# Kernel tuning notes

Measured on AMD Instinct MI355X. Metric: run time of the kernel, lower is better.

The kernel has to match this reference:

```python
import jax, jax.numpy as jnp
import numpy as np

B, S, D, H, FF = 4, 1024, 1024, 8, 4096
DK = D // H
EPS = 1e-5


def layernorm(x, g, b):
    m = jnp.mean(x, axis=-1, keepdims=True)
    v = jnp.mean(jnp.square(x - m), axis=-1, keepdims=True)
    return (x - m) * jax.lax.rsqrt(v + EPS) * g + b


def setup_inputs() -> dict:
    key = jax.random.key(0)
    ks = jax.random.split(key, 8)
    w = lambda k, shape: jax.random.normal(k, shape, jnp.float32) * 0.02
    return {
        "x": jax.random.normal(ks[0], (B, S, D), jnp.float32),
        "mask": jnp.ones((B, 1, 1, S), jnp.int32),  # unused in 'infer' mode, kept for fidelity
        "g1": jnp.ones((D,), jnp.float32), "b1": jnp.zeros((D,), jnp.float32),
        "Wq": w(ks[1], (D, D)), "bq": jnp.zeros((D,), jnp.float32),
        "Wk": w(ks[2], (D, D)), "bk": jnp.zeros((D,), jnp.float32),
        "Wv": w(ks[3], (D, H * D)), "bv": jnp.zeros((H * D,), jnp.float32),
        "g2": jnp.ones((D,), jnp.float32), "b2": jnp.zeros((D,), jnp.float32),
        "W1": w(ks[4], (D, FF)), "bw1": jnp.zeros((FF,), jnp.float32),
        "W2": w(ks[5], (FF, D)), "bw2": jnp.zeros((D,), jnp.float32),
    }


def reference(x, mask, g1, b1, Wq, bq, Wk, bk, Wv, bv, g2, b2, W1, bw1, W2, bw2):
    # --- MultiHeadedAttention (mode='infer'; mask is ignored by this path) ---
    xn = layernorm(x, g1, b1)                                   # [B,S,D]
    q = (xn @ Wq + bq).reshape(B, S, H, DK).transpose(0, 2, 1, 3)  # [B,H,S,DK]
    k = (xn @ Wk + bk).reshape(B, S, H, DK).transpose(0, 2, 1, 3)  # [B,H,S,DK]
    v = (xn @ Wv + bv).reshape(B, S, H, D).transpose(0, 2, 1, 3)   # [B,H,S,D]
    scores = jnp.einsum('bhqd,bhkd->bhqk', q, k) / jnp.sqrt(jnp.float32(DK))
    p = jax.nn.softmax(scores, axis=-1)                          # [B,H,S,S]
    ctx = jnp.einsum('bhqk,bhkd->bhqd', p, v)                    # [B,H,S,D]
    # Source does x.view(-1, B, dim, h).sum(heads).view(B, S, dim) on the
    # contiguous [B,H,S,D] tensor: a raw row-major reshape, reproduced exactly.
    attn_out = ctx.reshape(S, B, D, H).sum(axis=-1).reshape(B, S, D)
    # --- residual + SublayerConnection (pre-norm GELU FFN) ---
    x1 = x + attn_out
    xn2 = layernorm(x1, g2, b2)
    ffn = jax.nn.gelu(xn2 @ W1 + bw1, approximate=False) @ W2 + bw2
    return x1 + ffn
```

## Files before the change

kernel.cpp:

```cpp
#include <hip/hip_runtime.h>
#include <hip/hip_bf16.h>
#include <math.h>

typedef __attribute__((ext_vector_type(8))) short   short8;
typedef __attribute__((ext_vector_type(4))) short   short4v;
typedef __attribute__((ext_vector_type(8))) __bf16  bf16x8;
typedef __attribute__((ext_vector_type(4))) float   f32x4;

typedef const __attribute__((address_space(1))) void cgv_t;
typedef __attribute__((address_space(3))) void lv_t;

__device__ __forceinline__ float bs2f(short s) {
  unsigned int u = ((unsigned int)(unsigned short)s) << 16;
  return __builtin_bit_cast(float, u);
}
__device__ __forceinline__ short f2bs(float f) {
  __hip_bfloat16 h = __float2bfloat16(f);
  return __builtin_bit_cast(short, h);
}
__device__ __forceinline__ void glds16(const short* g, short* l) {
  __builtin_amdgcn_global_load_lds((cgv_t*)g, (lv_t*)l, 16, 0, 0);
}


__global__ __launch_bounds__(256) void transpose_k(const float* __restrict__ in,
                                                   short* __restrict__ out,
                                                   int R, int C) {
  __shared__ __align__(16) short T[64 * 72];
  const int r0 = blockIdx.y * 64, c0 = blockIdx.x * 64;
  const int t = threadIdx.x;
  {
    const int rr = t >> 4;
    const int cc = (t & 15) << 2;
#pragma unroll
    for (int h = 0; h < 4; h++) {
      const int row = rr + h * 16;
      f32x4 v = *(const f32x4*)(in + (long)(r0 + row) * C + c0 + cc);
#pragma unroll
      for (int e = 0; e < 4; e++) T[row * 72 + cc + e] = f2bs(v[e]);
    }
  }
  __syncthreads();
  {
    const int cr = t >> 3;
    const int rs = (t & 7) << 3;
#pragma unroll
    for (int h = 0; h < 2; h++) {
      const int c = cr + h * 32;
      short8 v;
#pragma unroll
      for (int e = 0; e < 8; e++) v[e] = T[(rs + e) * 72 + c];
      *(short8*)(out + (long)(c0 + c) * R + r0 + rs) = v;
    }
  }
}

__global__ __launch_bounds__(256) void wv8_k(const float* __restrict__ Wv,
                                             short* __restrict__ out) {
  __shared__ __align__(16) short T[64 * 72];
  const int r0 = blockIdx.x * 64, k0 = blockIdx.y * 64;
  const int t = threadIdx.x;
  const int wave = t >> 6, lane = t & 63;
  const int r = r0 + lane;
#pragma unroll 4
  for (int i = 0; i < 16; i++) {
    const int k = k0 + wave * 16 + i;
    const float* src = Wv + (long)k * 8192 + 8 * r;
    f32x4 a = *(const f32x4*)src;
    f32x4 b = *(const f32x4*)(src + 4);
    float s = (a[0] + a[1] + a[2] + a[3]) + (b[0] + b[1] + b[2] + b[3]);
    T[lane * 72 + wave * 16 + i] = f2bs(s);
  }
  __syncthreads();
  const int rr = t >> 3, kc = (t & 7) << 3;
#pragma unroll
  for (int half = 0; half < 2; half++) {
    const int rl = rr + half * 32;
    *(short8*)(out + (long)(r0 + rl) * 1024 + k0 + kc) = *(const short8*)&T[rl * 72 + kc];
  }
}

__global__ __launch_bounds__(256) void bv8_k(const float* __restrict__ bv,
                                             float* __restrict__ out) {
  const int r = blockIdx.x * 256 + threadIdx.x;
  f32x4 a = *(const f32x4*)(bv + 8 * r);
  f32x4 b = *(const f32x4*)(bv + 8 * r + 4);
  out[r] = (a[0] + a[1] + a[2] + a[3]) + (b[0] + b[1] + b[2] + b[3]);
}

__global__ __launch_bounds__(256) void ln_k(const float* __restrict__ in,
                                            const float* __restrict__ g,
                                            const float* __restrict__ b,
                                            short* __restrict__ out) {
  const int t = threadIdx.x;
  const long base = (long)blockIdx.x * 1024 + t * 4;
  f32x4 f = *(const f32x4*)(in + base);
  float v[4] = {f[0], f[1], f[2], f[3]};
  float s1 = v[0] + v[1] + v[2] + v[3];
  float s2 = v[0]*v[0] + v[1]*v[1] + v[2]*v[2] + v[3]*v[3];
#pragma unroll
  for (int off = 32; off; off >>= 1) {
    s1 += __shfl_xor(s1, off);
    s2 += __shfl_xor(s2, off);
  }
  __shared__ float rs[4], rq[4];
  if ((t & 63) == 0) { rs[t >> 6] = s1; rq[t >> 6] = s2; }
  __syncthreads();
  s1 = rs[0] + rs[1] + rs[2] + rs[3];
  s2 = rq[0] + rq[1] + rq[2] + rq[3];
  const float mean = s1 * (1.0f / 1024.0f);
  const float var  = s2 * (1.0f / 1024.0f) - mean * mean;
  const float rstd = rsqrtf(var + 1e-5f);
  f32x4 gv = *(const f32x4*)(g + t * 4);
  f32x4 bv = *(const f32x4*)(b + t * 4);
  short4v o;
#pragma unroll
  for (int i = 0; i < 4; i++)
    o[i] = f2bs((v[i] - mean) * rstd * gv[i] + bv[i]);
  *(short4v*)(out + base) = o;
}

__global__ __launch_bounds__(256) void reduce4_k(const float* __restrict__ p,
                                                 const float* __restrict__ x1,
                                                 const float* __restrict__ bias,
                                                 float* __restrict__ out) {
  const int t = threadIdx.x;
  const long base = (long)blockIdx.x * 1024 + t * 4;
  f32x4 a = *(const f32x4*)(p + base);
  f32x4 b = *(const f32x4*)(p + 4194304 + base);
  f32x4 c = *(const f32x4*)(p + 8388608 + base);
  f32x4 d = *(const f32x4*)(p + 12582912 + base);
  f32x4 e = *(const f32x4*)(x1 + base);
  f32x4 g = *(const f32x4*)(bias + t * 4);
  *(f32x4*)(out + base) = a + b + c + d + e + g;
}

__global__ __launch_bounds__(256, 2) void flash_k(
    const short* __restrict__ Qg_, const short* __restrict__ Kg_,
    const short* __restrict__ V8T, const float* __restrict__ xg,
    float* __restrict__ x1) {
  __shared__ __align__(16) short smem[40960];
  short* Qs = smem;
  short* Ks = smem + 8192;
  short* Vs = smem + 24576;

  const int t = threadIdx.x;
  const int wave = t >> 6, lane = t & 63;
  const int llo = lane & 15, lhi = lane >> 4;

  int lin = blockIdx.x + (blockIdx.y << 4);
  lin = (lin & 7) * 64 + (lin >> 3);
  const int q0 = (lin & 15) * 64;
  const int bh = lin >> 4, b = bh >> 3, h = bh & 7;

  const short* Qg = Qg_ + ((long)(b * 1024 + q0)) * 1024 + h * 128;
  const short* Kg = Kg_ + ((long)b * 1024) * 1024 + h * 128;
  const short* Vg = V8T + (long)bh * 131072;

  const int srow = t >> 2;
  const int sgc = (((t & 3) ^ ((t >> 3) & 3)) << 3);
  const int wbase = wave * 512;
  const int swzo = ((lhi ^ ((llo >> 1) & 3)) << 3);
  const int arow = (wave * 16 + llo) * 32 + swzo;

#pragma unroll
  for (int kk = 0; kk < 4; kk++)
    glds16(Qg + (long)srow * 1024 + kk * 32 + sgc, Qs + kk * 2048 + wbase);

  f32x4 o[8];
  float mR[4], lR[4];
#pragma unroll
  for (int i = 0; i < 8; i++) o[i] = f32x4{0.f, 0.f, 0.f, 0.f};
#pragma unroll
  for (int r = 0; r < 4; r++) { mR[r] = -1e30f; lR[r] = 0.f; }

  for (int it = 0; it < 8; it++) {
    const int kt0 = it * 128;
#pragma unroll
    for (int kk = 0; kk < 4; kk++) {
      glds16(Kg + (long)(kt0 + srow) * 1024 + kk * 32 + sgc,
             Ks + kk * 4096 + wbase);
      glds16(Kg + (long)(kt0 + 64 + srow) * 1024 + kk * 32 + sgc,
             Ks + kk * 4096 + 2048 + wbase);
      glds16(Vg + (long)srow * 1024 + kt0 + kk * 32 + sgc,
             Vs + kk * 4096 + wbase);
      glds16(Vg + (long)(64 + srow) * 1024 + kt0 + kk * 32 + sgc,
             Vs + kk * 4096 + 2048 + wbase);
    }
    __syncthreads();

    f32x4 s[8];
#pragma unroll
    for (int i = 0; i < 8; i++) s[i] = f32x4{0.f, 0.f, 0.f, 0.f};
#pragma unroll
    for (int kk = 0; kk < 4; kk++) {
      bf16x8 aq = *(const bf16x8*)(Qs + kk * 2048 + arow);
#pragma unroll
      for (int ct = 0; ct < 8; ct++) {
        bf16x8 bk = *(const bf16x8*)(Ks + kk * 4096 + (ct * 16 + llo) * 32 + swzo);
        s[ct] = __builtin_amdgcn_mfma_f32_16x16x32_bf16(aq, bk, s[ct], 0, 0, 0);
      }
    }
    float mt[4];
#pragma unroll
    for (int r = 0; r < 4; r++) {
      float m = s[0][r];
#pragma unroll
      for (int ct = 1; ct < 8; ct++) m = fmaxf(m, s[ct][r]);
      m = fmaxf(m, __shfl_xor(m, 1));
      m = fmaxf(m, __shfl_xor(m, 2));
      m = fmaxf(m, __shfl_xor(m, 4));
      m = fmaxf(m, __shfl_xor(m, 8));
      mt[r] = m;
    }
    bool need = (mt[0] > mR[0] + 8.f) | (mt[1] > mR[1] + 8.f) |
                (mt[2] > mR[2] + 8.f) | (mt[3] > mR[3] + 8.f);
    if (__any(need)) {
      float alpha[4];
#pragma unroll
      for (int r = 0; r < 4; r++) {
        const float mn = fmaxf(mR[r], mt[r]);
        alpha[r] = __builtin_amdgcn_exp2f(mR[r] - mn);
        mR[r] = mn;
        lR[r] *= alpha[r];
      }
#pragma unroll
      for (int ct = 0; ct < 8; ct++)
#pragma unroll
        for (int r = 0; r < 4; r++) o[ct][r] *= alpha[r];
    }
#pragma unroll
    for (int ct = 0; ct < 8; ct++)
#pragma unroll
      for (int r = 0; r < 4; r++)
        s[ct][r] = __builtin_amdgcn_exp2f(s[ct][r] - mR[r]);
#pragma unroll
    for (int r = 0; r < 4; r++) {
      float ls = s[0][r];
#pragma unroll
      for (int ct = 1; ct < 8; ct++) ls += s[ct][r];
      ls += __shfl_xor(ls, 1);
      ls += __shfl_xor(ls, 2);
      ls += __shfl_xor(ls, 4);
      ls += __shfl_xor(ls, 8);
      lR[r] += ls;
    }
    __syncthreads();

#pragma unroll
    for (int ct = 0; ct < 8; ct++) {
      const int chunk = ((ct & 1) << 1) | (llo >> 3);
      const int cl = llo & 7;
#pragma unroll
      for (int r = 0; r < 4; r++) {
        const int row = wave * 16 + lhi * 4 + r;
        const int xr = ((lhi << 1) | (r >> 1)) & 3;
        Ks[(ct >> 1) * 4096 + row * 32 + (((chunk ^ xr) << 3) | cl)] = f2bs(s[ct][r]);
      }
    }
    __syncthreads();

#pragma unroll
    for (int kk = 0; kk < 4; kk++) {
      bf16x8 ap = *(const bf16x8*)(Ks + kk * 4096 + arow);
#pragma unroll
      for (int ct = 0; ct < 8; ct++) {
        bf16x8 bv = *(const bf16x8*)(Vs + kk * 4096 + (ct * 16 + llo) * 32 + swzo);
        o[ct] = __builtin_amdgcn_mfma_f32_16x16x32_bf16(ap, bv, o[ct], 0, 0, 0);
      }
    }
    __syncthreads();
  }

  float inv[4];
#pragma unroll
  for (int r = 0; r < 4; r++) inv[r] = 1.0f / lR[r];
#pragma unroll
  for (int ct = 0; ct < 8; ct++) {
#pragma unroll
    for (int r = 0; r < 4; r++) {
      const int row = q0 + wave * 16 + lhi * 4 + r;
      const long idx = ((long)(b * 8 + h) * 1024 + row) * 128 + ct * 16 + llo;
      x1[idx] = xg[idx] + o[ct][r] * inv[r];
    }
  }
}

enum { E_GELU = 0, E_QKV = 1, E_PART = 2 };

#define MF16(va, vb, vc) __builtin_amdgcn_mfma_f32_16x16x32_bf16(va, vb, vc, 0, 0, 0)
#define VMW(n) asm volatile("s_waitcnt vmcnt(" #n ")" ::: "memory")
#define NOPS ((void)0)

#define STAGE_A(BUF, KH, KB) do {                                          \
    glds16(Ag + (KB), smem + ((BUF) * 2 + (KH)) * 8192 + wofs);            \
    glds16(Ag2 + (KB), smem + ((BUF) * 2 + (KH)) * 8192 + 4096 + wofs);    \
  } while (0)
#define STAGE_B(BUF, KH, KB) do {                                          \
    glds16(Bg + (KB), smem + 32768 + ((BUF) * 2 + (KH)) * 8192 + wofs);    \
    glds16(Bg2 + (KB), smem + 32768 + ((BUF) * 2 + (KH)) * 8192 + 4096 + wofs); \
  } while (0)

#define PHASE(RH, KH, BUF, LOADB, STAGE_STMT, WAIT_STMT)                   \
  {                                                                        \
    const short* Ar_ = smem + ((BUF) * 2 + (KH)) * 8192 + aoff + (RH) * 2048; \
    bf16x8 a0 = *(const bf16x8*)(Ar_);                                     \
    bf16x8 a1 = *(const bf16x8*)(Ar_ + 512);                               \
    bf16x8 a2 = *(const bf16x8*)(Ar_ + 1024);                              \
    bf16x8 a3 = *(const bf16x8*)(Ar_ + 1536);                              \
    if (LOADB) {                                                           \
      const short* Br_ = smem + 32768 + ((BUF) * 2 + (KH)) * 8192 + boff;  \
      vb0 = *(const bf16x8*)(Br_);                                         \
      vb1 = *(const bf16x8*)(Br_ + 512);                                   \
      vb2 = *(const bf16x8*)(Br_ + 1024);                                  \
      vb3 = *(const bf16x8*)(Br_ + 1536);                                  \
    }                                                                      \
    STAGE_STMT;                                                            \
    __builtin_amdgcn_s_setprio(1);                                         \
    acc[(RH) * 4 + 0][0] = MF16(a0, vb0, acc[(RH) * 4 + 0][0]);            \
    acc[(RH) * 4 + 0][1] = MF16(a0, vb1, acc[(RH) * 4 + 0][1]);            \
    acc[(RH) * 4 + 0][2] = MF16(a0, vb2, acc[(RH) * 4 + 0][2]);            \
    acc[(RH) * 4 + 0][3] = MF16(a0, vb3, acc[(RH) * 4 + 0][3]);            \
    acc[(RH) * 4 + 1][0] = MF16(a1, vb0, acc[(RH) * 4 + 1][0]);            \
    acc[(RH) * 4 + 1][1] = MF16(a1, vb1, acc[(RH) * 4 + 1][1]);            \
    acc[(RH) * 4 + 1][2] = MF16(a1, vb2, acc[(RH) * 4 + 1][2]);            \
    acc[(RH) * 4 + 1][3] = MF16(a1, vb3, acc[(RH) * 4 + 1][3]);            \
    acc[(RH) * 4 + 2][0] = MF16(a2, vb0, acc[(RH) * 4 + 2][0]);            \
    acc[(RH) * 4 + 2][1] = MF16(a2, vb1, acc[(RH) * 4 + 2][1]);            \
    acc[(RH) * 4 + 2][2] = MF16(a2, vb2, acc[(RH) * 4 + 2][2]);            \
    acc[(RH) * 4 + 2][3] = MF16(a2, vb3, acc[(RH) * 4 + 2][3]);            \
    acc[(RH) * 4 + 3][0] = MF16(a3, vb0, acc[(RH) * 4 + 3][0]);            \
    acc[(RH) * 4 + 3][1] = MF16(a3, vb1, acc[(RH) * 4 + 3][1]);            \
    acc[(RH) * 4 + 3][2] = MF16(a3, vb2, acc[(RH) * 4 + 3][2]);            \
    acc[(RH) * 4 + 3][3] = MF16(a3, vb3, acc[(RH) * 4 + 3][3]);            \
    __builtin_amdgcn_s_setprio(0);                                         \
    WAIT_STMT;                                                             \
    __builtin_amdgcn_sched_barrier(0);                                     \
    __builtin_amdgcn_s_barrier();                                          \
    __builtin_amdgcn_sched_barrier(0);                                     \
  }

#define TILE8(T, BUF)                                                        \
  PHASE(0, 0, BUF, 1, STAGE_A(1 - (BUF), 1, ((T) + 1) * 64 + 32), NOPS);     \
  PHASE(1, 0, BUF, 0, STAGE_B(1 - (BUF), 1, ((T) + 1) * 64 + 32), VMW(8));   \
  PHASE(0, 1, BUF, 1, STAGE_A(BUF, 0, ((T) + 2) * 64), NOPS);                \
  PHASE(1, 1, BUF, 0, STAGE_B(BUF, 0, ((T) + 2) * 64), VMW(8))

template <int EPI>
__global__ __launch_bounds__(512, 2) void gemm256(
    const short* __restrict__ A, int lda, long azk,
    const short* __restrict__ Bt, int ldb, long bzk,
    const float* __restrict__ bias, long biasl,
    void* __restrict__ outp, long czl, int ldc,
    void* __restrict__ aux, int K) {
  __shared__ __align__(16) short smem[65536];

  const int t = threadIdx.x;
  const int wave = t >> 6, lane = t & 63;
  const int llo = lane & 15, lhi = lane >> 4;
  const int wm = wave >> 2, wn = wave & 3;

  int lin = blockIdx.x + gridDim.x * (blockIdx.y + gridDim.y * blockIdx.z);
  const int nwg = gridDim.x * gridDim.y * gridDim.z;
  lin = (lin & 7) * (nwg >> 3) + (lin >> 3);
  const int bx = lin % gridDim.x;
  const int rem = lin / gridDim.x;
  const int by = rem % gridDim.y;
  const int z = rem / gridDim.y;

  const int bm0 = by * 256, bn0 = bx * 256;
  A += (long)z * azk;
  Bt += (long)z * bzk;

  const int srow = t >> 2;
  const int sgc = (((t & 3) ^ ((t >> 3) & 3)) << 3);
  const short* Ag  = A  + (long)(bm0 + srow) * lda + sgc;
  const short* Ag2 = A  + (long)(bm0 + 128 + srow) * lda + sgc;
  const short* Bg  = Bt + (long)(bn0 + srow) * ldb + sgc;
  const short* Bg2 = Bt + (long)(bn0 + 128 + srow) * ldb + sgc;
  const int wofs = wave * 512;

  const int swz = ((lhi ^ ((llo >> 1) & 3)) << 3);
  const int aoff = (wm * 128 + llo) * 32 + swz;
  const int boff = (wn * 64 + llo) * 32 + swz;

  f32x4 acc[8][4];
#pragma unroll
  for (int i = 0; i < 8; i++)
#pragma unroll
    for (int j = 0; j < 4; j++) acc[i][j] = f32x4{0.f, 0.f, 0.f, 0.f};
  bf16x8 vb0, vb1, vb2, vb3;

  const int NT = K >> 6;

  STAGE_A(0, 0, 0);  STAGE_B(0, 0, 0);
  STAGE_A(0, 1, 32); STAGE_B(0, 1, 32);
  STAGE_A(1, 0, 64); STAGE_B(1, 0, 64);
  VMW(8);
  __builtin_amdgcn_sched_barrier(0);
  __builtin_amdgcn_s_barrier();
  __builtin_amdgcn_sched_barrier(0);

  for (int tt = 0; tt < NT - 2; tt += 2) {
    TILE8(tt, 0);
    TILE8(tt + 1, 1);
  }
  PHASE(0, 0, 0, 1, STAGE_A(1, 1, (NT - 1) * 64 + 32), NOPS);
  PHASE(1, 0, 0, 0, STAGE_B(1, 1, (NT - 1) * 64 + 32), VMW(8));
  PHASE(0, 1, 0, 1, NOPS, NOPS);
  PHASE(1, 1, 0, 0, NOPS, VMW(4));
  PHASE(0, 0, 1, 1, NOPS, NOPS);
  PHASE(1, 0, 1, 0, NOPS, VMW(0));
  PHASE(0, 1, 1, 1, NOPS, NOPS);
  PHASE(1, 1, 1, 0, NOPS, NOPS);

  if (EPI == E_PART) {
    float* P = (float*)outp + (long)z * czl;
#pragma unroll
    for (int ct = 0; ct < 4; ct++) {
      const int col = bn0 + wn * 64 + ct * 16 + llo;
#pragma unroll
      for (int rt = 0; rt < 8; rt++) {
#pragma unroll
        for (int r = 0; r < 4; r++) {
          const int row = bm0 + wm * 128 + rt * 16 + lhi * 4 + r;
          P[(long)row * ldc + col] = acc[rt][ct][r];
        }
      }
    }
  } else if (EPI == E_QKV && z == 2) {
    short* slab = smem + wave * 4352;
    const int bb = bm0 >> 10, sbase = (bm0 & 1023) + wm * 128;
    float bv4[4];
#pragma unroll
    for (int ct = 0; ct < 4; ct++)
      bv4[ct] = bias[z * biasl + bn0 + wn * 64 + ct * 16 + llo];
    const int gcol = bn0 + wn * 64 + lane;
    short* dst0 = (short*)aux + ((long)(bb * 8 + (gcol >> 7))) * 131072 +
                  (long)(gcol & 127) * 1024 + sbase;
#pragma unroll
    for (int p = 0; p < 2; p++) {
#pragma unroll
      for (int rt4 = 0; rt4 < 4; rt4++) {
#pragma unroll
        for (int ct = 0; ct < 4; ct++) {
#pragma unroll
          for (int r = 0; r < 4; r++) {
            float v = acc[p * 4 + rt4][ct][r] + bv4[ct];
            slab[(ct * 16 + llo) * 68 + rt4 * 16 + lhi * 4 + r] = f2bs(v);
          }
        }
      }
#pragma unroll
      for (int j = 0; j < 8; j++)
        *(short8*)(dst0 + p * 64 + j * 8) = *(const short8*)&slab[lane * 68 + j * 8];
    }
  } else {
    short* C = (short*)outp + (long)z * czl;
    short* slab = smem + wave * 4864;
    float bv4[4];
#pragma unroll
    for (int ct = 0; ct < 4; ct++)
      bv4[ct] = bias[z * biasl + bn0 + wn * 64 + ct * 16 + llo];
    const int rl0 = lane >> 3, cb8 = (lane & 7) << 3;
    const short* srd = slab + rl0 * 76 + cb8;
    short* Cw = C + (long)(bm0 + wm * 128 + rl0) * ldc + bn0 + wn * 64 + cb8;
#pragma unroll
    for (int p = 0; p < 2; p++) {
#pragma unroll
      for (int rt4 = 0; rt4 < 4; rt4++) {
#pragma unroll
        for (int ct = 0; ct < 4; ct++) {
#pragma unroll
          for (int r = 0; r < 4; r++) {
            float v = acc[p * 4 + rt4][ct][r] + bv4[ct];
            if (EPI == E_GELU)
              v = 0.5f * v * (1.0f + erff(v * 0.70710678118654752f));
            if (EPI == E_QKV && z == 0)
              v *= 0.12751744476582f;
            slab[(rt4 * 16 + lhi * 4 + r) * 76 + ct * 16 + llo] = f2bs(v);
          }
        }
      }
#pragma unroll
      for (int j = 0; j < 8; j++) {
        short8 v = *(const short8*)(srd + j * 8 * 76);
        *(short8*)(Cw + ((long)p * 64 + j * 8) * ldc) = v;
      }
    }
  }
}

extern "C" void kernel_launch(void* const* d_in, const int* in_sizes, int n_in,
                              void* d_out, int out_size, void* d_ws, size_t ws_size,
                              hipStream_t stream) {
  const float* x   = (const float*)d_in[0];
  const float* g1  = (const float*)d_in[2];
  const float* b1  = (const float*)d_in[3];
  const float* Wq  = (const float*)d_in[4];
  const float* bq  = (const float*)d_in[5];
  const float* Wk  = (const float*)d_in[6];
  const float* bk  = (const float*)d_in[7];
  const float* Wv  = (const float*)d_in[8];
  const float* bv  = (const float*)d_in[9];
  const float* g2  = (const float*)d_in[10];
  const float* b2  = (const float*)d_in[11];
  const float* W1  = (const float*)d_in[12];
  const float* bw1 = (const float*)d_in[13];
  const float* W2  = (const float*)d_in[14];
  const float* bw2 = (const float*)d_in[15];

  char* ws = (char*)d_ws;
  const long MB = 1024 * 1024;
  float* bQKV  = (float*)(ws);
  float* x1    = (float*)(ws + 1 * MB);
  short* wqT   = (short*)(ws + 17 * MB);
  short* wkT   = (short*)(ws + 19 * MB);
  short* wv8T  = (short*)(ws + 21 * MB);
  short* xn    = (short*)(ws + 23 * MB);
  short* Q     = (short*)(ws + 31 * MB);
  short* Kb    = (short*)(ws + 39 * MB);
  short* V8T   = (short*)(ws + 47 * MB);
  short* xn2  = (short*)(ws + 17 * MB);
  short* Hb   = (short*)(ws + 25 * MB);
  short* w1T  = (short*)(ws + 57 * MB);
  short* w2T  = (short*)(ws + 65 * MB);
  float* part = (float*)(ws + 73 * MB);

  hipMemcpyAsync(bQKV, bq, 4096, hipMemcpyDeviceToDevice, stream);
  hipMemcpyAsync(bQKV + 1024, bk, 4096, hipMemcpyDeviceToDevice, stream);
  bv8_k<<<4, 256, 0, stream>>>(bv, bQKV + 2048);

  transpose_k<<<dim3(16, 16), 256, 0, stream>>>(Wq, wqT, 1024, 1024);
  transpose_k<<<dim3(16, 16), 256, 0, stream>>>(Wk, wkT, 1024, 1024);
  wv8_k<<<dim3(16, 16), 256, 0, stream>>>(Wv, wv8T);

  ln_k<<<4096, 256, 0, stream>>>(x, g1, b1, xn);

  gemm256<E_QKV><<<dim3(4, 16, 3), 512, 0, stream>>>(
      xn, 1024, 0, wqT, 1024, 1048576, bQKV, 1024,
      Q, 4194304, 1024, V8T, 1024);

  flash_k<<<dim3(16, 32), 256, 0, stream>>>(Q, Kb, V8T, x, x1);

  transpose_k<<<dim3(64, 16), 256, 0, stream>>>(W1, w1T, 1024, 4096);
  transpose_k<<<dim3(16, 64), 256, 0, stream>>>(W2, w2T, 4096, 1024);

  ln_k<<<4096, 256, 0, stream>>>(x1, g2, b2, xn2);

  gemm256<E_GELU><<<dim3(16, 16, 1), 512, 0, stream>>>(
      xn2, 1024, 0, w1T, 1024, 0, bw1, 0,
      Hb, 0, 4096, nullptr, 1024);

  gemm256<E_PART><<<dim3(4, 16, 4), 512, 0, stream>>>(
      Hb, 4096, 1024, w2T, 4096, 1024, nullptr, 0,
      part, 4194304, 1024, nullptr, 1024);

  reduce4_k<<<4096, 256, 0, stream>>>(part, x1, bw2, (float*)d_out);
}
```

Baseline: 358.4 us.

## Merge prep kernels into one launch and fold residual plus bias into GEMM epilogue

The separate bias copies, bias-sum, weight transposes (Wq, Wk, Wv-reduce, W1, W2) and the first layernorm are folded into a single prep_k launch. It dispatches on block index, so the many small launches and their serialization gaps go away. The W1/W2 transposes move ahead of attention into this launch. The residual x1 and the bw2 bias are now added in the split-K GEMM epilogue of the z==0 slice. That lets the final reduction read only the four partials. The trade-off is extra uncoalesced-ish loads of x1 in one GEMM slice's epilogue, plus a heterogeneous grid whose blocks do different amounts of work.

```diff
diff --git a/kernel.cpp b/kernel.cpp
--- a/kernel.cpp
+++ b/kernel.cpp
@@ -23,11 +23,11 @@
 }
 
 
-__global__ __launch_bounds__(256) void transpose_k(const float* __restrict__ in,
-                                                   short* __restrict__ out,
-                                                   int R, int C) {
-  __shared__ __align__(16) short T[64 * 72];
-  const int r0 = blockIdx.y * 64, c0 = blockIdx.x * 64;
+__device__ __forceinline__ void tr_body(const float* __restrict__ in,
+                                        short* __restrict__ out,
+                                        int R, int C, int bx, int by,
+                                        short* T) {
+  const int r0 = by * 64, c0 = bx * 64;
   const int t = threadIdx.x;
   {
     const int rr = t >> 4;
@@ -55,10 +55,10 @@
   }
 }
 
-__global__ __launch_bounds__(256) void wv8_k(const float* __restrict__ Wv,
-                                             short* __restrict__ out) {
-  __shared__ __align__(16) short T[64 * 72];
-  const int r0 = blockIdx.x * 64, k0 = blockIdx.y * 64;
+__device__ __forceinline__ void wv8_body(const float* __restrict__ Wv,
+                                         short* __restrict__ out,
+                                         int bx, int by, short* T) {
+  const int r0 = bx * 64, k0 = by * 64;
   const int t = threadIdx.x;
   const int wave = t >> 6, lane = t & 63;
   const int r = r0 + lane;
@@ -80,20 +80,13 @@
   }
 }
 
-__global__ __launch_bounds__(256) void bv8_k(const float* __restrict__ bv,
-                                             float* __restrict__ out) {
-  const int r = blockIdx.x * 256 + threadIdx.x;
-  f32x4 a = *(const f32x4*)(bv + 8 * r);
-  f32x4 b = *(const f32x4*)(bv + 8 * r + 4);
-  out[r] = (a[0] + a[1] + a[2] + a[3]) + (b[0] + b[1] + b[2] + b[3]);
-}
-
-__global__ __launch_bounds__(256) void ln_k(const float* __restrict__ in,
-                                            const float* __restrict__ g,
-                                            const float* __restrict__ b,
-                                            short* __restrict__ out) {
-  const int t = threadIdx.x;
-  const long base = (long)blockIdx.x * 1024 + t * 4;
+__device__ __forceinline__ void ln_body(const float* __restrict__ in,
+                                        const float* __restrict__ g,
+                                        const float* __restrict__ b,
+                                        short* __restrict__ out, int row,
+                                        float* rs, float* rq) {
+  const int t = threadIdx.x;
+  const long base = (long)row * 1024 + t * 4;
   f32x4 f = *(const f32x4*)(in + base);
   float v[4] = {f[0], f[1], f[2], f[3]};
   float s1 = v[0] + v[1] + v[2] + v[3];
@@ -103,7 +96,6 @@
     s1 += __shfl_xor(s1, off);
     s2 += __shfl_xor(s2, off);
   }
-  __shared__ float rs[4], rq[4];
   if ((t & 63) == 0) { rs[t >> 6] = s1; rq[t >> 6] = s2; }
   __syncthreads();
   s1 = rs[0] + rs[1] + rs[2] + rs[3];
@@ -120,9 +112,53 @@
   *(short4v*)(out + base) = o;
 }
 
+__global__ __launch_bounds__(256) void prep_k(
+    const float* __restrict__ x, const float* __restrict__ g1,
+    const float* __restrict__ b1, short* __restrict__ xn,
+    const float* __restrict__ Wq, short* __restrict__ wqT,
+    const float* __restrict__ Wk, short* __restrict__ wkT,
+    const float* __restrict__ Wv, short* __restrict__ wv8T,
+    const float* __restrict__ W1, short* __restrict__ w1T,
+    const float* __restrict__ W2, short* __restrict__ w2T,
+    const float* __restrict__ bq, const float* __restrict__ bk,
+    const float* __restrict__ bv, float* __restrict__ bQKV) {
+  __shared__ __align__(16) short T[64 * 72];
+  __shared__ float rs[4], rq[4];
+  const int t = threadIdx.x;
+  int bid = blockIdx.x;
+  if (bid < 4096) { ln_body(x, g1, b1, xn, bid, rs, rq); return; }
+  bid -= 4096;
+  if (bid < 256) { tr_body(Wq, wqT, 1024, 1024, bid & 15, bid >> 4, T); return; }
+  bid -= 256;
+  if (bid < 256) { tr_body(Wk, wkT, 1024, 1024, bid & 15, bid >> 4, T); return; }
+  bid -= 256;
+  if (bid < 256) { wv8_body(Wv, wv8T, bid & 15, bid >> 4, T); return; }
+  bid -= 256;
+  if (bid < 1024) { tr_body(W1, w1T, 1024, 4096, bid & 63, bid >> 6, T); return; }
+  bid -= 1024;
+  if (bid < 1024) { tr_body(W2, w2T, 4096, 1024, bid & 15, bid >> 4, T); return; }
+  bid -= 1024;
+  if (bid < 4) {
+    const int r = bid * 256 + t;
+    f32x4 a = *(const f32x4*)(bv + 8 * r);
+    f32x4 b = *(const f32x4*)(bv + 8 * r + 4);
+    bQKV[2048 + r] = (a[0] + a[1] + a[2] + a[3]) + (b[0] + b[1] + b[2] + b[3]);
+    return;
+  }
+  bid -= 4;
+  if (bid == 0) { *(f32x4*)(bQKV + t * 4) = *(const f32x4*)(bq + t * 4); }
+  else          { *(f32x4*)(bQKV + 1024 + t * 4) = *(const f32x4*)(bk + t * 4); }
+}
+
+__global__ __launch_bounds__(256) void ln_k(const float* __restrict__ in,
+                                            const float* __restrict__ g,
+                                            const float* __restrict__ b,
+                                            short* __restrict__ out) {
+  __shared__ float rs[4], rq[4];
+  ln_body(in, g, b, out, blockIdx.x, rs, rq);
+}
+
 __global__ __launch_bounds__(256) void reduce4_k(const float* __restrict__ p,
-                                                 const float* __restrict__ x1,
-                                                 const float* __restrict__ bias,
                                                  float* __restrict__ out) {
   const int t = threadIdx.x;
   const long base = (long)blockIdx.x * 1024 + t * 4;
@@ -130,9 +166,7 @@
   f32x4 b = *(const f32x4*)(p + 4194304 + base);
   f32x4 c = *(const f32x4*)(p + 8388608 + base);
   f32x4 d = *(const f32x4*)(p + 12582912 + base);
-  f32x4 e = *(const f32x4*)(x1 + base);
-  f32x4 g = *(const f32x4*)(bias + t * 4);
-  *(f32x4*)(out + base) = a + b + c + d + e + g;
+  *(f32x4*)(out + base) = a + b + c + d;
 }
 
 __global__ __launch_bounds__(256, 2) void flash_k(
@@ -416,15 +450,20 @@
 
   if (EPI == E_PART) {
     float* P = (float*)outp + (long)z * czl;
+    const float* x1p = (const float*)aux;
+    const bool add0 = (z == 0);
 #pragma unroll
     for (int ct = 0; ct < 4; ct++) {
       const int col = bn0 + wn * 64 + ct * 16 + llo;
+      const float bval = add0 ? bias[col] : 0.f;
 #pragma unroll
       for (int rt = 0; rt < 8; rt++) {
 #pragma unroll
         for (int r = 0; r < 4; r++) {
           const int row = bm0 + wm * 128 + rt * 16 + lhi * 4 + r;
-          P[(long)row * ldc + col] = acc[rt][ct][r];
+          float v = acc[rt][ct][r];
+          if (add0) v += x1p[(long)row * 1024 + col] + bval;
+          P[(long)row * ldc + col] = v;
         }
       }
     }
@@ -527,15 +566,10 @@
   short* w2T  = (short*)(ws + 65 * MB);
   float* part = (float*)(ws + 73 * MB);
 
-  hipMemcpyAsync(bQKV, bq, 4096, hipMemcpyDeviceToDevice, stream);
-  hipMemcpyAsync(bQKV + 1024, bk, 4096, hipMemcpyDeviceToDevice, stream);
-  bv8_k<<<4, 256, 0, stream>>>(bv, bQKV + 2048);
-
-  transpose_k<<<dim3(16, 16), 256, 0, stream>>>(Wq, wqT, 1024, 1024);
-  transpose_k<<<dim3(16, 16), 256, 0, stream>>>(Wk, wkT, 1024, 1024);
-  wv8_k<<<dim3(16, 16), 256, 0, stream>>>(Wv, wv8T);
-
-  ln_k<<<4096, 256, 0, stream>>>(x, g1, b1, xn);
+  prep_k<<<6918, 256, 0, stream>>>(x, g1, b1, xn,
+                                   Wq, wqT, Wk, wkT, Wv, wv8T,
+                                   W1, w1T, W2, w2T,
+                                   bq, bk, bv, bQKV);
 
   gemm256<E_QKV><<<dim3(4, 16, 3), 512, 0, stream>>>(
       xn, 1024, 0, wqT, 1024, 1048576, bQKV, 1024,
@@ -543,9 +577,6 @@
 
   flash_k<<<dim3(16, 32), 256, 0, stream>>>(Q, Kb, V8T, x, x1);
 
-  transpose_k<<<dim3(64, 16), 256, 0, stream>>>(W1, w1T, 1024, 4096);
-  transpose_k<<<dim3(16, 64), 256, 0, stream>>>(W2, w2T, 4096, 1024);
-
   ln_k<<<4096, 256, 0, stream>>>(x1, g2, b2, xn2);
 
   gemm256<E_GELU><<<dim3(16, 16, 1), 512, 0, stream>>>(
@@ -553,8 +584,8 @@
       Hb, 0, 4096, nullptr, 1024);
 
   gemm256<E_PART><<<dim3(4, 16, 4), 512, 0, stream>>>(
-      Hb, 4096, 1024, w2T, 4096, 1024, nullptr, 0,
-      part, 4194304, 1024, nullptr, 1024);
-
-  reduce4_k<<<4096, 256, 0, stream>>>(part, x1, bw2, (float*)d_out);
-}
+      Hb, 4096, 1024, w2T, 4096, 1024, bw2, 0,
+      part, 4194304, 1024, x1, 1024);
+
+  reduce4_k<<<4096, 256, 0, stream>>>(part, (float*)d_out);
+}
```

Measured after the change: 372.7 us. 4.0% more time.
